# Kernel tuning notes

Measured on AMD Instinct MI355X. Metric: run time of the kernel, lower is better.

The kernel has to match this reference:

```python
import jax, jax.numpy as jnp
import numpy as np

B, H, W, DIM, NH, HD = 2, 64, 160, 256, 8, 32
R0, R1 = 1, 1                      # win_r (x, y)
WX, WY = 2 * R0 + 2, 2 * R1 + 2    # window extents
A = WX * WY                        # attn_num = 16
SCALE = HD ** (-0.5)


def setup_inputs() -> dict:
    key = jax.random.key(0)
    ks = jax.random.split(key, 6)
    x = jax.random.normal(ks[0], (B, H, W, DIM), jnp.float32)
    # float match positions anywhere in the image; clamp in reference() keeps windows in-bounds
    u = jax.random.uniform(ks[1], (B, H * W, 2), jnp.float32)
    max_offset = u * jnp.array([W, H], jnp.float32)
    Wq = jax.random.normal(ks[2], (DIM, NH * HD), jnp.float32) * 0.02
    Wk = jax.random.normal(ks[3], (DIM, NH * HD), jnp.float32) * 0.02
    Wv = jax.random.normal(ks[4], (DIM, NH * HD), jnp.float32) * 0.02
    Wproj = jax.random.normal(ks[5], (NH * HD, DIM), jnp.float32) * 0.02
    return dict(x=x, max_offset=max_offset, Wq=Wq, Wk=Wk, Wv=Wv, Wproj=Wproj)


def reference(x, max_offset, Wq, Wk, Wv, Wproj):
    b, h, w, _ = x.shape
    n = h * w
    xf = x.reshape(b, n, -1)
    q = (xf @ Wq).reshape(b, n, NH, HD)
    k = (xf @ Wk).reshape(b, n, NH, HD)
    v = (xf @ Wv).reshape(b, n, NH, HD)

    # clamp_max_offset: keep the (2r+2)^2 window fully inside the image
    ox = jnp.clip(max_offset[..., 0], R0, w - 1 - R0 - 0.001)
    oy = jnp.clip(max_offset[..., 1], R1, h - 1 - R1 - 0.001)
    mx, my = jnp.floor(ox), jnp.floor(oy)
    fx, fy = ox - mx, oy - my  # bilinear fractions

    # window gather indices: rows my-R1..my+R1+1, cols mx-R0..mx+R0+1
    ix = mx.astype(jnp.int32)[..., None] + jnp.arange(-R0, R0 + 2)  # (b,n,WX)
    iy = my.astype(jnp.int32)[..., None] + jnp.arange(-R1, R1 + 2)  # (b,n,WY)
    idx = (iy[:, :, :, None] * w + ix[:, :, None, :]).reshape(b, n, A)  # (b,n,A)

    gather = jax.vmap(lambda t, i: t[i])  # per-batch row gather
    kg = gather(k.reshape(b, n, NH * HD), idx).reshape(b, n, A, NH, HD)
    vg = gather(v.reshape(b, n, NH * HD), idx).reshape(b, n, A, NH, HD)

    attn = jnp.einsum('bnhd,bnahd->bnha', q, kg) * SCALE  # (b,n,NH,A)

    # bilinear weights: edge elements weighted by (1-f)/f, interior by 1
    wx = jnp.concatenate([(1 - fx)[..., None], jnp.ones((b, n, 2 * R0), fx.dtype), fx[..., None]], axis=-1)
    wy = jnp.concatenate([(1 - fy)[..., None], jnp.ones((b, n, 2 * R1), fy.dtype), fy[..., None]], axis=-1)
    bw = (wy[:, :, :, None] * wx[:, :, None, :]).reshape(b, n, 1, A)

    # bilinear-weighted stable softmax
    m = jnp.max(attn, axis=-1, keepdims=True)
    e = jnp.exp(attn - m) * bw
    p = e / jnp.sum(e, axis=-1, keepdims=True)

    out = jnp.einsum('bnha,bnahd->bnhd', p, vg).reshape(b, n, NH * HD)
    out = out @ Wproj
    return out.reshape(b, h, w, -1)
```

## Files before the change

### kernel.cpp

```cpp
#include <hip/hip_runtime.h>
#include <math.h>

#define Bb   2
#define Hh   64
#define Ww   160
#define DIMc 256
#define NHh  8
#define Nn   (Hh * Ww)
#define SCALEf 0.17677669529663687f

typedef unsigned short u16;
typedef unsigned int   u32;
typedef __bf16 bf16x8 __attribute__((ext_vector_type(8)));
typedef float  f32x4  __attribute__((ext_vector_type(4)));

__device__ __forceinline__ u16 f2bf(float f) {
    u32 u = __float_as_uint(f);
    u += 0x7fffu + ((u >> 16) & 1u);
    return (u16)(u >> 16);
}
__device__ __forceinline__ float bflo(u32 u) { return __uint_as_float(u << 16); }
__device__ __forceinline__ float bfhi(u32 u) { return __uint_as_float(u & 0xffff0000u); }

__global__ __launch_bounds__(256) void convert_x(const float* __restrict__ x,
                                                 u16* __restrict__ xb)
{
    size_t id = (size_t)blockIdx.x * 256 + threadIdx.x;
    float4 vv = *(const float4*)(x + id * 4);
    ushort4 ov = make_ushort4(f2bf(vv.x), f2bf(vv.y), f2bf(vv.z), f2bf(vv.w));
    *(ushort4*)(xb + id * 4) = ov;
}

__global__ __launch_bounds__(256) void convert_w(const float* __restrict__ Wq,
                                                 const float* __restrict__ Wk,
                                                 const float* __restrict__ Wv,
                                                 const float* __restrict__ Wp,
                                                 u16* __restrict__ WtAll)
{
    int id = blockIdx.x * 256 + threadIdx.x;
    int wsel = id >> 16;
    int rem  = id & 65535;
    int k = rem >> 8, n = rem & 255;
    const float* W = (wsel == 0) ? Wq : (wsel == 1) ? Wk : (wsel == 2) ? Wv : Wp;
    WtAll[(size_t)wsel * 65536 + n * 256 + k] = f2bf(W[k * 256 + n]);
}

template <bool BF16OUT>
__device__ __forceinline__ void gemm_core(const u16* __restrict__ Ag,
                                          const u16* __restrict__ Btg,
                                          u16* __restrict__ Cb,
                                          float* __restrict__ Cf)
{
    __shared__ u16 sA[128 * 32];
    __shared__ u16 sB[128 * 32];

    const int t    = threadIdx.x;
    const int lane = t & 63;
    const int wv   = t >> 6;
    const int wm   = wv & 1;
    const int wn   = wv >> 1;
    const int m0   = blockIdx.y * 128;
    const int n0   = blockIdx.x * 128;

    const int r0  = t >> 2;
    const int kc0 = (t & 3) * 8;

    const int col  = lane & 15;
    const int quad = lane >> 4;

    f32x4 acc[4][4];
#pragma unroll
    for (int i = 0; i < 4; ++i)
#pragma unroll
        for (int j = 0; j < 4; ++j)
            acc[i][j] = (f32x4){0.f, 0.f, 0.f, 0.f};

    const u16* Abase = Ag + (size_t)m0 * 256;
    const u16* Bbase = Btg + (size_t)n0 * 256;

    for (int k0 = 0; k0 < 256; k0 += 32) {
        uint4 a0 = *(const uint4*)(Abase + (size_t)r0 * 256 + k0 + kc0);
        uint4 a1 = *(const uint4*)(Abase + (size_t)(64 + r0) * 256 + k0 + kc0);
        uint4 b0 = *(const uint4*)(Bbase + (size_t)r0 * 256 + k0 + kc0);
        uint4 b1 = *(const uint4*)(Bbase + (size_t)(64 + r0) * 256 + k0 + kc0);
        __syncthreads();
        *(uint4*)(sA + r0 * 32 + kc0)        = a0;
        *(uint4*)(sA + (64 + r0) * 32 + kc0) = a1;
        *(uint4*)(sB + r0 * 32 + kc0)        = b0;
        *(uint4*)(sB + (64 + r0) * 32 + kc0) = b1;
        __syncthreads();

        bf16x8 af[4], bfr[4];
#pragma unroll
        for (int mt = 0; mt < 4; ++mt)
            af[mt] = *(const bf16x8*)(sA + (wm * 64 + mt * 16 + col) * 32 + quad * 8);
#pragma unroll
        for (int nt = 0; nt < 4; ++nt)
            bfr[nt] = *(const bf16x8*)(sB + (wn * 64 + nt * 16 + col) * 32 + quad * 8);

#pragma unroll
        for (int mt = 0; mt < 4; ++mt)
#pragma unroll
            for (int nt = 0; nt < 4; ++nt)
                acc[mt][nt] = __builtin_amdgcn_mfma_f32_16x16x32_bf16(af[mt], bfr[nt], acc[mt][nt], 0, 0, 0);
    }

#pragma unroll
    for (int mt = 0; mt < 4; ++mt) {
#pragma unroll
        for (int nt = 0; nt < 4; ++nt) {
            const int rowb = m0 + wm * 64 + mt * 16 + quad * 4;
            const int colg = n0 + wn * 64 + nt * 16 + col;
#pragma unroll
            for (int rr = 0; rr < 4; ++rr) {
                float val = acc[mt][nt][rr];
                if (BF16OUT) Cb[(size_t)(rowb + rr) * 256 + colg] = f2bf(val);
                else         Cf[(size_t)(rowb + rr) * 256 + colg] = val;
            }
        }
    }
}

__global__ __launch_bounds__(256) void gemm_qkv(const u16* __restrict__ xb,
                                                const u16* __restrict__ WtAll,
                                                u16* __restrict__ q,
                                                u16* __restrict__ k,
                                                u16* __restrict__ v)
{
    const int z = blockIdx.z;
    u16* C = (z == 0) ? q : (z == 1) ? k : v;
    gemm_core<true>(xb, WtAll + (size_t)z * 65536, C, nullptr);
}

__global__ __launch_bounds__(256) void gemm_proj(const u16* __restrict__ ao,
                                                 const u16* __restrict__ WtAll,
                                                 float* __restrict__ out)
{
    gemm_core<false>(ao, WtAll + (size_t)3 * 65536, nullptr, out);
}

__global__ __launch_bounds__(128) void attn_kernel(const u16* __restrict__ q,
                                                   const u16* __restrict__ k,
                                                   const u16* __restrict__ v,
                                                   const float* __restrict__ moff,
                                                   u16* __restrict__ out)
{
    const int pos  = blockIdx.x;
    const int t    = threadIdx.x;
    const int brow = (pos >= Nn) ? Nn : 0;

    __shared__ float qs[256];
    __shared__ int   idxS[16];
    __shared__ float bwS[16];
    __shared__ float scores[8][16];
    __shared__ float pS[8][16];

    u32 qw = *(const u32*)(q + (size_t)pos * 256 + 2 * t);
    qs[2 * t]     = bflo(qw);
    qs[2 * t + 1] = bfhi(qw);

    if (t == 0) {
        float ox = moff[(size_t)pos * 2 + 0];
        float oy = moff[(size_t)pos * 2 + 1];
        ox = fminf(fmaxf(ox, 1.0f), (float)(Ww - 2) - 0.001f);
        oy = fminf(fmaxf(oy, 1.0f), (float)(Hh - 2) - 0.001f);
        float mxf = floorf(ox), myf = floorf(oy);
        float fx = ox - mxf, fy = oy - myf;
        int imx = (int)mxf, imy = (int)myf;
        float wxv[4] = {1.0f - fx, 1.0f, 1.0f, fx};
        float wyv[4] = {1.0f - fy, 1.0f, 1.0f, fy};
#pragma unroll
        for (int r = 0; r < 4; ++r)
#pragma unroll
            for (int c = 0; c < 4; ++c) {
                idxS[r * 4 + c] = (imy + r - 1) * Ww + (imx + c - 1);
                bwS[r * 4 + c]  = wyv[r] * wxv[c];
            }
    }
    __syncthreads();

    {
        const int h = t >> 4, a = t & 15;
        const uint4* kp = (const uint4*)(k + ((size_t)(brow + idxS[a])) * 256 + h * 32);
        float s = 0.f;
#pragma unroll
        for (int jj = 0; jj < 4; ++jj) {
            uint4 w4 = kp[jj];
            const float* qh = qs + h * 32 + jj * 8;
            s += qh[0] * bflo(w4.x) + qh[1] * bfhi(w4.x)
               + qh[2] * bflo(w4.y) + qh[3] * bfhi(w4.y)
               + qh[4] * bflo(w4.z) + qh[5] * bfhi(w4.z)
               + qh[6] * bflo(w4.w) + qh[7] * bfhi(w4.w);
        }
        scores[h][a] = s * SCALEf;
    }
    __syncthreads();

    if (t < 8) {
        float m = -INFINITY;
#pragma unroll
        for (int a = 0; a < 16; ++a) m = fmaxf(m, scores[t][a]);
        float e[16];
        float sum = 0.f;
#pragma unroll
        for (int a = 0; a < 16; ++a) {
            e[a] = expf(scores[t][a] - m) * bwS[a];
            sum += e[a];
        }
        float inv = 1.0f / sum;
#pragma unroll
        for (int a = 0; a < 16; ++a) pS[t][a] = e[a] * inv;
    }
    __syncthreads();

    {
        const int h = t >> 4;
        float acc0 = 0.f, acc1 = 0.f;
#pragma unroll
        for (int a = 0; a < 16; ++a) {
            u32 w2 = *(const u32*)(v + ((size_t)(brow + idxS[a])) * 256 + 2 * t);
            float p = pS[h][a];
            acc0 += p * bflo(w2);
            acc1 += p * bfhi(w2);
        }
        u32 packed = ((u32)f2bf(acc1) << 16) | (u32)f2bf(acc0);
        *(u32*)(out + (size_t)pos * 256 + 2 * t) = packed;
    }
}

extern "C" void kernel_launch(void* const* d_in, const int* in_sizes, int n_in,
                              void* d_out, int out_size, void* d_ws, size_t ws_size,
                              hipStream_t stream)
{
    const float* x     = (const float*)d_in[0];
    const float* moff  = (const float*)d_in[1];
    const float* Wq    = (const float*)d_in[2];
    const float* Wk    = (const float*)d_in[3];
    const float* Wv    = (const float*)d_in[4];
    const float* Wproj = (const float*)d_in[5];
    float* out = (float*)d_out;

    const size_t NTOT = (size_t)Bb * Nn * DIMc;
    u16* ws    = (u16*)d_ws;
    u16* xb    = ws;
    u16* WtAll = xb + NTOT;
    u16* q     = WtAll + 4 * 65536;
    u16* k     = q + NTOT;
    u16* v     = k + NTOT;
    u16* ao    = v + NTOT;

    convert_x<<<dim3((int)(NTOT / 4 / 256)), dim3(256), 0, stream>>>(x, xb);
    convert_w<<<dim3(1024), dim3(256), 0, stream>>>(Wq, Wk, Wv, Wproj, WtAll);
    gemm_qkv<<<dim3(2, 160, 3), dim3(256), 0, stream>>>(xb, WtAll, q, k, v);
    attn_kernel<<<dim3(Bb * Nn), dim3(128), 0, stream>>>(q, k, v, moff, ao);
    gemm_proj<<<dim3(2, 160, 1), dim3(256), 0, stream>>>(ao, WtAll, out);
}
```

Baseline: 149.7 us.

## Merge conversion kernels, widen GEMM N-tile, and rewrite attention as wave-per-position

The two input-conversion kernels become one launch. The GEMMs now use a 128x256 tile, so each block covers the full output width and loads A only once. The attention kernel now processes one query position per wavefront, four per block. It replaces shared-memory staging and block barriers with register-held q, shuffle reductions for the softmax, and wider V loads. The change cuts launch count, barrier overhead and redundant A traffic, at the cost of fewer GEMM blocks (160 blocks total for the projection) and higher register pressure.

```diff
diff --git a/kernel.cpp b/kernel.cpp
--- a/kernel.cpp
+++ b/kernel.cpp
@@ -5,7 +5,6 @@
 #define Hh   64
 #define Ww   160
 #define DIMc 256
-#define NHh  8
 #define Nn   (Hh * Ww)
 #define SCALEf 0.17677669529663687f
 
@@ -19,98 +18,109 @@
     u += 0x7fffu + ((u >> 16) & 1u);
     return (u16)(u >> 16);
 }
+__device__ __forceinline__ u32 pack2(float lo, float hi) {
+    return (u32)f2bf(lo) | ((u32)f2bf(hi) << 16);
+}
 __device__ __forceinline__ float bflo(u32 u) { return __uint_as_float(u << 16); }
 __device__ __forceinline__ float bfhi(u32 u) { return __uint_as_float(u & 0xffff0000u); }
 
-__global__ __launch_bounds__(256) void convert_x(const float* __restrict__ x,
-                                                 u16* __restrict__ xb)
-{
-    size_t id = (size_t)blockIdx.x * 256 + threadIdx.x;
-    float4 vv = *(const float4*)(x + id * 4);
-    ushort4 ov = make_ushort4(f2bf(vv.x), f2bf(vv.y), f2bf(vv.z), f2bf(vv.w));
-    *(ushort4*)(xb + id * 4) = ov;
-}
-
-__global__ __launch_bounds__(256) void convert_w(const float* __restrict__ Wq,
-                                                 const float* __restrict__ Wk,
-                                                 const float* __restrict__ Wv,
-                                                 const float* __restrict__ Wp,
-                                                 u16* __restrict__ WtAll)
-{
-    int id = blockIdx.x * 256 + threadIdx.x;
-    int wsel = id >> 16;
-    int rem  = id & 65535;
-    int k = rem >> 8, n = rem & 255;
-    const float* W = (wsel == 0) ? Wq : (wsel == 1) ? Wk : (wsel == 2) ? Wv : Wp;
-    WtAll[(size_t)wsel * 65536 + n * 256 + k] = f2bf(W[k * 256 + n]);
+__global__ __launch_bounds__(256) void prep(const float* __restrict__ x,
+                                            const float* __restrict__ Wq,
+                                            const float* __restrict__ Wk,
+                                            const float* __restrict__ Wv,
+                                            const float* __restrict__ Wp,
+                                            u16* __restrict__ xb,
+                                            u16* __restrict__ WtAll)
+{
+    const int bid = blockIdx.x;
+    if (bid < 5120) {
+        size_t id = (size_t)bid * 256 + threadIdx.x;
+        float4 vv = *(const float4*)(x + id * 4);
+        ushort4 ov = make_ushort4(f2bf(vv.x), f2bf(vv.y), f2bf(vv.z), f2bf(vv.w));
+        *(ushort4*)(xb + id * 4) = ov;
+    } else {
+        int id = (bid - 5120) * 256 + threadIdx.x;
+        int wsel = id >> 16;
+        int rem  = id & 65535;
+        int kk = rem >> 8, nn = rem & 255;
+        const float* W = (wsel == 0) ? Wq : (wsel == 1) ? Wk : (wsel == 2) ? Wv : Wp;
+        WtAll[(size_t)wsel * 65536 + nn * 256 + kk] = f2bf(W[kk * 256 + nn]);
+    }
 }
 
 template <bool BF16OUT>
-__device__ __forceinline__ void gemm_core(const u16* __restrict__ Ag,
-                                          const u16* __restrict__ Btg,
-                                          u16* __restrict__ Cb,
-                                          float* __restrict__ Cf)
+__device__ __forceinline__ void gemm_core256(const u16* __restrict__ Ag,
+                                             const u16* __restrict__ Btg,
+                                             u16* __restrict__ Cb,
+                                             float* __restrict__ Cf,
+                                             int m0)
 {
     __shared__ u16 sA[128 * 32];
-    __shared__ u16 sB[128 * 32];
+    __shared__ u16 sB[256 * 32];
 
     const int t    = threadIdx.x;
     const int lane = t & 63;
     const int wv   = t >> 6;
     const int wm   = wv & 1;
     const int wn   = wv >> 1;
-    const int m0   = blockIdx.y * 128;
-    const int n0   = blockIdx.x * 128;
-
-    const int r0  = t >> 2;
-    const int kc0 = (t & 3) * 8;
-
     const int col  = lane & 15;
     const int quad = lane >> 4;
 
-    f32x4 acc[4][4];
+    f32x4 acc[4][8];
 #pragma unroll
     for (int i = 0; i < 4; ++i)
 #pragma unroll
-        for (int j = 0; j < 4; ++j)
+        for (int j = 0; j < 8; ++j)
             acc[i][j] = (f32x4){0.f, 0.f, 0.f, 0.f};
 
     const u16* Abase = Ag + (size_t)m0 * 256;
-    const u16* Bbase = Btg + (size_t)n0 * 256;
 
     for (int k0 = 0; k0 < 256; k0 += 32) {
-        uint4 a0 = *(const uint4*)(Abase + (size_t)r0 * 256 + k0 + kc0);
-        uint4 a1 = *(const uint4*)(Abase + (size_t)(64 + r0) * 256 + k0 + kc0);
-        uint4 b0 = *(const uint4*)(Bbase + (size_t)r0 * 256 + k0 + kc0);
-        uint4 b1 = *(const uint4*)(Bbase + (size_t)(64 + r0) * 256 + k0 + kc0);
+        uint4 av[2], bv[4];
+#pragma unroll
+        for (int i = 0; i < 2; ++i) {
+            int c = i * 256 + t, r = c >> 2, kc = (c & 3) * 8;
+            av[i] = *(const uint4*)(Abase + (size_t)r * 256 + k0 + kc);
+        }
+#pragma unroll
+        for (int i = 0; i < 4; ++i) {
+            int c = i * 256 + t, r = c >> 2, kc = (c & 3) * 8;
+            bv[i] = *(const uint4*)(Btg + (size_t)r * 256 + k0 + kc);
+        }
         __syncthreads();
-        *(uint4*)(sA + r0 * 32 + kc0)        = a0;
-        *(uint4*)(sA + (64 + r0) * 32 + kc0) = a1;
-        *(uint4*)(sB + r0 * 32 + kc0)        = b0;
-        *(uint4*)(sB + (64 + r0) * 32 + kc0) = b1;
+#pragma unroll
+        for (int i = 0; i < 2; ++i) {
+            int c = i * 256 + t, r = c >> 2, kc = (c & 3) * 8;
+            *(uint4*)(sA + r * 32 + kc) = av[i];
+        }
+#pragma unroll
+        for (int i = 0; i < 4; ++i) {
+            int c = i * 256 + t, r = c >> 2, kc = (c & 3) * 8;
+            *(uint4*)(sB + r * 32 + kc) = bv[i];
+        }
         __syncthreads();
 
-        bf16x8 af[4], bfr[4];
+        bf16x8 af[4], bfr[8];
 #pragma unroll
         for (int mt = 0; mt < 4; ++mt)
             af[mt] = *(const bf16x8*)(sA + (wm * 64 + mt * 16 + col) * 32 + quad * 8);
 #pragma unroll
-        for (int nt = 0; nt < 4; ++nt)
-            bfr[nt] = *(const bf16x8*)(sB + (wn * 64 + nt * 16 + col) * 32 + quad * 8);
+        for (int nt = 0; nt < 8; ++nt)
+            bfr[nt] = *(const bf16x8*)(sB + (wn * 128 + nt * 16 + col) * 32 + quad * 8);
 
 #pragma unroll
         for (int mt = 0; mt < 4; ++mt)
 #pragma unroll
-            for (int nt = 0; nt < 4; ++nt)
+            for (int nt = 0; nt < 8; ++nt)
                 acc[mt][nt] = __builtin_amdgcn_mfma_f32_16x16x32_bf16(af[mt], bfr[nt], acc[mt][nt], 0, 0, 0);
     }
 
 #pragma unroll
     for (int mt = 0; mt < 4; ++mt) {
 #pragma unroll
-        for (int nt = 0; nt < 4; ++nt) {
+        for (int nt = 0; nt < 8; ++nt) {
             const int rowb = m0 + wm * 64 + mt * 16 + quad * 4;
-            const int colg = n0 + wn * 64 + nt * 16 + col;
+            const int colg = wn * 128 + nt * 16 + col;
 #pragma unroll
             for (int rr = 0; rr < 4; ++rr) {
                 float val = acc[mt][nt][rr];
@@ -121,111 +131,102 @@
     }
 }
 
-__global__ __launch_bounds__(256) void gemm_qkv(const u16* __restrict__ xb,
-                                                const u16* __restrict__ WtAll,
-                                                u16* __restrict__ q,
-                                                u16* __restrict__ k,
-                                                u16* __restrict__ v)
-{
-    const int z = blockIdx.z;
+__global__ __launch_bounds__(256, 2) void gemm_qkv(const u16* __restrict__ xb,
+                                                   const u16* __restrict__ WtAll,
+                                                   u16* __restrict__ q,
+                                                   u16* __restrict__ k,
+                                                   u16* __restrict__ v)
+{
+    const int z = blockIdx.y;
     u16* C = (z == 0) ? q : (z == 1) ? k : v;
-    gemm_core<true>(xb, WtAll + (size_t)z * 65536, C, nullptr);
-}
-
-__global__ __launch_bounds__(256) void gemm_proj(const u16* __restrict__ ao,
-                                                 const u16* __restrict__ WtAll,
-                                                 float* __restrict__ out)
-{
-    gemm_core<false>(ao, WtAll + (size_t)3 * 65536, nullptr, out);
-}
-
-__global__ __launch_bounds__(128) void attn_kernel(const u16* __restrict__ q,
+    gemm_core256<true>(xb, WtAll + (size_t)z * 65536, C, nullptr, blockIdx.x * 128);
+}
+
+__global__ __launch_bounds__(256, 2) void gemm_proj(const u16* __restrict__ ao,
+                                                    const u16* __restrict__ WtAll,
+                                                    float* __restrict__ out)
+{
+    gemm_core256<false>(ao, WtAll + (size_t)3 * 65536, nullptr, out, blockIdx.x * 128);
+}
+
+__global__ __launch_bounds__(256) void attn_kernel(const u16* __restrict__ q,
                                                    const u16* __restrict__ k,
                                                    const u16* __restrict__ v,
                                                    const float* __restrict__ moff,
-                                                   u16* __restrict__ out)
-{
-    const int pos  = blockIdx.x;
-    const int t    = threadIdx.x;
-    const int brow = (pos >= Nn) ? Nn : 0;
-
-    __shared__ float qs[256];
-    __shared__ int   idxS[16];
-    __shared__ float bwS[16];
-    __shared__ float scores[8][16];
-    __shared__ float pS[8][16];
-
-    u32 qw = *(const u32*)(q + (size_t)pos * 256 + 2 * t);
-    qs[2 * t]     = bflo(qw);
-    qs[2 * t + 1] = bfhi(qw);
-
-    if (t == 0) {
-        float ox = moff[(size_t)pos * 2 + 0];
-        float oy = moff[(size_t)pos * 2 + 1];
-        ox = fminf(fmaxf(ox, 1.0f), (float)(Ww - 2) - 0.001f);
-        oy = fminf(fmaxf(oy, 1.0f), (float)(Hh - 2) - 0.001f);
-        float mxf = floorf(ox), myf = floorf(oy);
-        float fx = ox - mxf, fy = oy - myf;
-        int imx = (int)mxf, imy = (int)myf;
-        float wxv[4] = {1.0f - fx, 1.0f, 1.0f, fx};
-        float wyv[4] = {1.0f - fy, 1.0f, 1.0f, fy};
-#pragma unroll
-        for (int r = 0; r < 4; ++r)
-#pragma unroll
-            for (int c = 0; c < 4; ++c) {
-                idxS[r * 4 + c] = (imy + r - 1) * Ww + (imx + c - 1);
-                bwS[r * 4 + c]  = wyv[r] * wxv[c];
-            }
-    }
-    __syncthreads();
-
+                                                   u16* __restrict__ ao)
+{
+    const int wv   = threadIdx.x >> 6;
+    const int lane = threadIdx.x & 63;
+    const int pos  = blockIdx.x * 4 + wv;
+    const int rowbase = (pos >= Nn) ? Nn : 0;
+
+    float2 mo = *(const float2*)(moff + (size_t)pos * 2);
+    float ox = fminf(fmaxf(mo.x, 1.0f), (float)(Ww - 2) - 0.001f);
+    float oy = fminf(fmaxf(mo.y, 1.0f), (float)(Hh - 2) - 0.001f);
+    float mxf = floorf(ox), myf = floorf(oy);
+    float fx = ox - mxf, fy = oy - myf;
+    int imx = (int)mxf, imy = (int)myf;
+
+    const int h  = lane & 7;
+    const int a0 = lane >> 3;
+
+    uint4 q4[4];
     {
-        const int h = t >> 4, a = t & 15;
-        const uint4* kp = (const uint4*)(k + ((size_t)(brow + idxS[a])) * 256 + h * 32);
-        float s = 0.f;
+        const uint4* qp = (const uint4*)(q + (size_t)pos * 256 + h * 32);
+#pragma unroll
+        for (int jj = 0; jj < 4; ++jj) q4[jj] = qp[jj];
+    }
+
+    float s[2];
+#pragma unroll
+    for (int p = 0; p < 2; ++p) {
+        int a   = a0 + 8 * p;
+        int row = rowbase + (imy + (a >> 2) - 1) * Ww + imx + (a & 3) - 1;
+        const uint4* kp = (const uint4*)(k + (size_t)row * 256 + h * 32);
+        float acc = 0.f;
 #pragma unroll
         for (int jj = 0; jj < 4; ++jj) {
-            uint4 w4 = kp[jj];
-            const float* qh = qs + h * 32 + jj * 8;
-            s += qh[0] * bflo(w4.x) + qh[1] * bfhi(w4.x)
-               + qh[2] * bflo(w4.y) + qh[3] * bfhi(w4.y)
-               + qh[4] * bflo(w4.z) + qh[5] * bfhi(w4.z)
-               + qh[6] * bflo(w4.w) + qh[7] * bfhi(w4.w);
-        }
-        scores[h][a] = s * SCALEf;
-    }
-    __syncthreads();
-
-    if (t < 8) {
-        float m = -INFINITY;
-#pragma unroll
-        for (int a = 0; a < 16; ++a) m = fmaxf(m, scores[t][a]);
-        float e[16];
-        float sum = 0.f;
-#pragma unroll
-        for (int a = 0; a < 16; ++a) {
-            e[a] = expf(scores[t][a] - m) * bwS[a];
-            sum += e[a];
-        }
-        float inv = 1.0f / sum;
-#pragma unroll
-        for (int a = 0; a < 16; ++a) pS[t][a] = e[a] * inv;
-    }
-    __syncthreads();
-
-    {
-        const int h = t >> 4;
-        float acc0 = 0.f, acc1 = 0.f;
-#pragma unroll
-        for (int a = 0; a < 16; ++a) {
-            u32 w2 = *(const u32*)(v + ((size_t)(brow + idxS[a])) * 256 + 2 * t);
-            float p = pS[h][a];
-            acc0 += p * bflo(w2);
-            acc1 += p * bfhi(w2);
-        }
-        u32 packed = ((u32)f2bf(acc1) << 16) | (u32)f2bf(acc0);
-        *(u32*)(out + (size_t)pos * 256 + 2 * t) = packed;
-    }
+            uint4 kw = kp[jj];
+            acc += bflo(q4[jj].x) * bflo(kw.x) + bfhi(q4[jj].x) * bfhi(kw.x)
+                 + bflo(q4[jj].y) * bflo(kw.y) + bfhi(q4[jj].y) * bfhi(kw.y)
+                 + bflo(q4[jj].z) * bflo(kw.z) + bfhi(q4[jj].z) * bfhi(kw.z)
+                 + bflo(q4[jj].w) * bflo(kw.w) + bfhi(q4[jj].w) * bfhi(kw.w);
+        }
+        s[p] = acc * SCALEf;
+    }
+
+    auto wc = [](int r, float f) { return r == 0 ? 1.f - f : (r == 3 ? f : 1.f); };
+    float bw0 = wc(a0 >> 2, fy) * wc(a0 & 3, fx);
+    float bw1 = wc((a0 + 8) >> 2, fy) * wc(a0 & 3, fx);
+
+    float m = fmaxf(s[0], s[1]);
+    m = fmaxf(m, __shfl_xor(m, 8));
+    m = fmaxf(m, __shfl_xor(m, 16));
+    m = fmaxf(m, __shfl_xor(m, 32));
+    float e0 = expf(s[0] - m) * bw0;
+    float e1 = expf(s[1] - m) * bw1;
+    float sum = e0 + e1;
+    sum += __shfl_xor(sum, 8);
+    sum += __shfl_xor(sum, 16);
+    sum += __shfl_xor(sum, 32);
+    float inv = 1.f / sum;
+    float p0 = e0 * inv, p1 = e1 * inv;
+
+    float acc0 = 0.f, acc1 = 0.f, acc2 = 0.f, acc3 = 0.f;
+    const int myh = lane >> 3;
+#pragma unroll
+    for (int a = 0; a < 16; ++a) {
+        int row = rowbase + (imy + (a >> 2) - 1) * Ww + imx + (a & 3) - 1;
+        uint2 vw = *(const uint2*)(v + (size_t)row * 256 + 4 * lane);
+        int src = ((a & 7) << 3) | myh;
+        float pa = __shfl(a < 8 ? p0 : p1, src);
+        acc0 += pa * bflo(vw.x); acc1 += pa * bfhi(vw.x);
+        acc2 += pa * bflo(vw.y); acc3 += pa * bfhi(vw.y);
+    }
+    uint2 o;
+    o.x = pack2(acc0, acc1);
+    o.y = pack2(acc2, acc3);
+    *(uint2*)(ao + (size_t)pos * 256 + 4 * lane) = o;
 }
 
 extern "C" void kernel_launch(void* const* d_in, const int* in_sizes, int n_in,
@@ -249,9 +250,8 @@
     u16* v     = k + NTOT;
     u16* ao    = v + NTOT;
 
-    convert_x<<<dim3((int)(NTOT / 4 / 256)), dim3(256), 0, stream>>>(x, xb);
-    convert_w<<<dim3(1024), dim3(256), 0, stream>>>(Wq, Wk, Wv, Wproj, WtAll);
-    gemm_qkv<<<dim3(2, 160, 3), dim3(256), 0, stream>>>(xb, WtAll, q, k, v);
-    attn_kernel<<<dim3(Bb * Nn), dim3(128), 0, stream>>>(q, k, v, moff, ao);
-    gemm_proj<<<dim3(2, 160, 1), dim3(256), 0, stream>>>(ao, WtAll, out);
-}
+    prep<<<dim3(6144), dim3(256), 0, stream>>>(x, Wq, Wk, Wv, Wproj, xb, WtAll);
+    gemm_qkv<<<dim3(160, 3), dim3(256), 0, stream>>>(xb, WtAll, q, k, v);
+    attn_kernel<<<dim3(Bb * Nn / 4), dim3(256), 0, stream>>>(q, k, v, moff, ao);
+    gemm_proj<<<dim3(160), dim3(256), 0, stream>>>(ao, WtAll, out);
+}
```

Result: slower. 181.5 us (+21.2%).
